# Performance work log

Hardware: AMD Instinct MI355X
Metric: run time of the kernel (lower is better)

## Reference

```python
import jax, jax.numpy as jnp
import numpy as np

B, T, P, D, H = 32, 64, 196, 768, 12
HD = D // H   # MHA head dim = 64
F = D // H    # GAT per-head out features = 64


def _grid_adj(num_patches):
    g = int(np.sqrt(num_patches))
    a = np.zeros((num_patches, num_patches), np.int32)
    for i in range(num_patches):
        a[i, i] = 1
        r, c = divmod(i, g)
        for dr in (-1, 0, 1):
            for dc in (-1, 0, 1):
                if dr == 0 and dc == 0:
                    continue
                nr, nc = r + dr, c + dc
                if 0 <= nr < g and 0 <= nc < g:
                    a[i, nr * g + nc] = 1
    return a


def setup_inputs():
    key = jax.random.key(0)
    ks = jax.random.split(key, 32)
    s = 0.02
    ta = jax.random.randint(ks[2], (B, T, T), 0, 2).astype(jnp.int32)
    ta = jnp.maximum(jnp.maximum(ta, ta.transpose(0, 2, 1)), jnp.eye(T, dtype=jnp.int32))
    return {
        'text_features': jax.random.normal(ks[0], (B, T, D), jnp.float32),
        'image_features': jax.random.normal(ks[1], (B, P, D), jnp.float32),
        'clip_text': jax.random.normal(ks[3], (B, 512), jnp.float32),
        'clip_image': jax.random.normal(ks[4], (B, 512), jnp.float32),
        'logit_scale': jnp.float32(4.6052),  # ln(100), CLIP default
        'wq': jax.random.normal(ks[5], (D, D), jnp.float32) * s,
        'bq': jnp.zeros((D,), jnp.float32),
        'wk': jax.random.normal(ks[6], (D, D), jnp.float32) * s,
        'bk': jnp.zeros((D,), jnp.float32),
        'wv': jax.random.normal(ks[7], (D, D), jnp.float32) * s,
        'bv': jnp.zeros((D,), jnp.float32),
        'wo': jax.random.normal(ks[8], (D, D), jnp.float32) * s,
        'bo': jnp.zeros((D,), jnp.float32),
        'Wt': jax.random.normal(ks[9], (D, H * F), jnp.float32) * s,
        'at': jax.random.normal(ks[10], (2 * F, 1), jnp.float32) * s,
        'Wi': jax.random.normal(ks[11], (D, H * F), jnp.float32) * s,
        'ai': jax.random.normal(ks[12], (2 * F, 1), jnp.float32) * s,
        'Wp': jax.random.normal(ks[13], (512, D), jnp.float32) * s,
        'bp': jnp.zeros((D,), jnp.float32),
        'f1w': jax.random.normal(ks[14], (3, 16), jnp.float32) * 0.3,
        'f1b': jnp.zeros((16,), jnp.float32),
        'f2w': jax.random.normal(ks[15], (16, 3), jnp.float32) * 0.3,
        'f2b': jnp.zeros((3,), jnp.float32),
        'c1w': jax.random.normal(ks[16], (D, D // 2), jnp.float32) * s,
        'c1b': jnp.zeros((D // 2,), jnp.float32),
        'c2w': jax.random.normal(ks[17], (D // 2, 2), jnp.float32) * s,
        'c2b': jnp.zeros((2,), jnp.float32),
        'text_adj': ta,
        'image_adj': jnp.asarray(_grid_adj(P)),
    }


def _gat(h, adj, W, a):
    # h: [N, D], adj: [N, N] (0/1), W: [D, H*F], a: [2F, 1]
    N = h.shape[0]
    Wh = (h @ W).reshape(N, H, F)
    # e_ij = leakyrelu(a^T [Wh_i ; Wh_j]) decomposed to avoid the N*N*2F concat tensor
    src = jnp.einsum('nhf,f->nh', Wh, a[:F, 0])   # [N, H]
    dst = jnp.einsum('nhf,f->nh', Wh, a[F:, 0])   # [N, H]
    e = jax.nn.leaky_relu(src[:, None, :] + dst[None, :, :], 0.2)  # [N, N, H]
    e = jnp.where(adj[:, :, None] > 0, e, jnp.float32(-9e15))
    att = jax.nn.softmax(e, axis=1)               # softmax over neighbors j
    hp = jnp.einsum('ijh,jhf->ihf', att, Wh)       # [N, H, F]
    return jax.nn.elu(hp.reshape(N, H * F))


def reference(text_features, image_features, clip_text, clip_image, logit_scale,
              wq, bq, wk, bk, wv, bv, wo, bo, Wt, at, Wi, ai, Wp, bp,
              f1w, f1b, f2w, f2b, c1w, c1b, c2w, c2b, text_adj, image_adj):
    # token-level cross attention (text queries, image keys/values)
    q = (text_features @ wq + bq).reshape(B, T, H, HD)
    k = (image_features @ wk + bk).reshape(B, P, H, HD)
    v = (image_features @ wv + bv).reshape(B, P, H, HD)
    scores = jnp.einsum('bthd,bphd->bhtp', q, k) / jnp.sqrt(jnp.float32(HD))
    upd = jnp.einsum('bhtp,bphd->bthd', jax.nn.softmax(scores, axis=-1), v)
    upd = upd.reshape(B, T, D) @ wo + bo           # [B, T, D]
    c = jnp.einsum('btd,bpd->btp', upd, image_features)
    s_token = jnp.mean(jnp.diagonal(c, axis1=-2, axis2=-1), axis=1)  # [B]
    f_token = upd.mean(axis=1)                     # [B, D]
    # per-sample GATs, batched via vmap
    tg = jax.vmap(lambda h, a_: _gat(h, a_, Wt, at))(text_features, text_adj)
    ig = jax.vmap(lambda h: _gat(h, image_adj, Wi, ai))(image_features)
    tgf = tg.mean(axis=1)
    igf = ig.mean(axis=1)

    def cos(x, y):
        nx = jnp.maximum(jnp.linalg.norm(x, axis=-1), 1e-8)
        ny = jnp.maximum(jnp.linalg.norm(y, axis=-1), 1e-8)
        return jnp.sum(x * y, axis=-1) / (nx * ny)

    s_phrase = cos(tgf, igf)
    s_global = jnp.exp(logit_scale) * cos(clip_text, clip_image)
    f_global = clip_text @ Wp + bp
    scores3 = jax.lax.stop_gradient(jnp.stack([s_token, s_phrase, s_global], axis=1))
    w = jax.nn.sigmoid(jax.nn.gelu(scores3 @ f1w + f1b, approximate=False) @ f2w + f2b)
    f_agg = w[:, 0:1] * f_token + w[:, 1:2] * tgf + w[:, 2:3] * f_global
    logits = jax.nn.relu(f_agg @ c1w + c1b) @ c2w + c2b  # dropout inactive (eval)
    return logits
```

## Files before the change

kernel.cpp:

```cpp
#include <hip/hip_runtime.h>
#include <hip/hip_bf16.h>
#include <math.h>

#define B 32
#define T 64
#define P 196
#define D 768
#define H 12

typedef __attribute__((ext_vector_type(8))) short short8;
typedef __attribute__((ext_vector_type(4))) float floatx4;

__device__ __forceinline__ float wave_sum(float v) {
#pragma unroll
  for (int o = 32; o > 0; o >>= 1) v += __shfl_xor(v, o);
  return v;
}
__device__ __forceinline__ unsigned short f2bf(float x) {
  unsigned u = __float_as_uint(x);
  u += 0x7FFFu + ((u >> 16) & 1u);
  return (unsigned short)(u >> 16);
}
__device__ __forceinline__ float bf2f(unsigned short x) {
  return __uint_as_float((unsigned)x << 16);
}
__device__ __forceinline__ float fexp(float x) { return __expf(x); }
__device__ __forceinline__ float frcp(float x) { return __builtin_amdgcn_rcpf(x); }
__device__ __forceinline__ void async_cp16(const unsigned short* g, unsigned short* l) {
  __builtin_amdgcn_global_load_lds(
      (const __attribute__((address_space(1))) unsigned int*)g,
      (__attribute__((address_space(3))) unsigned int*)l, 16, 0, 0);
}
__device__ __forceinline__ int xcd_remap(int orig, int nwg) {
  const int q = nwg >> 3, r = nwg & 7;
  const int x = orig & 7, o = orig >> 3;
  return (x < r ? x * (q + 1) : r * (q + 1) + (x - r) * q) + o;
}

struct WPack {
  const float* src[6];
  unsigned short* dst[6];
};
__global__ __launch_bounds__(256) void prep_kernel(
    WPack p,
    const float* __restrict__ text, unsigned short* __restrict__ text_bf, int n40,
    const float* __restrict__ img, unsigned short* __restrict__ img_bf, int n41,
    const float* __restrict__ bq, const float* __restrict__ bk,
    const float* __restrict__ bv,
    float* __restrict__ bt, float* __restrict__ bi, float* __restrict__ stok) {
  const int bid = blockIdx.x;
  if (bid < 3456) {
    __shared__ float tile[32][33];
    const int z = bid / 576, rem = bid % 576;
    const int bx = rem % 24, by = rem / 24;
    const float* W = p.src[z];
    unsigned short* Wt = p.dst[z];
    const int tx = threadIdx.x & 31, ty = threadIdx.x >> 5;
    const int n0 = bx * 32, k0 = by * 32;
#pragma unroll
    for (int r = 0; r < 4; ++r)
      tile[ty + 8 * r][tx] = W[(size_t)(k0 + ty + 8 * r) * D + n0 + tx];
    __syncthreads();
#pragma unroll
    for (int r = 0; r < 4; ++r)
      Wt[(size_t)(n0 + ty + 8 * r) * D + k0 + tx] = f2bf(tile[tx][ty + 8 * r]);
  } else if (bid < 9696) {
    int i = (bid - 3456) * 256 + threadIdx.x;
    const float* X;
    unsigned short* Y;
    int idx;
    if (i < n40) { X = text; Y = text_bf; idx = i; }
    else if (i < n40 + n41) { X = img; Y = img_bf; idx = i - n40; }
    else return;
    float4 vv = ((const float4*)X)[idx];
    ushort4 o;
    o.x = f2bf(vv.x); o.y = f2bf(vv.y); o.z = f2bf(vv.z); o.w = f2bf(vv.w);
    ((ushort4*)Y)[idx] = o;
  } else {
    int i = (bid - 9696) * 256 + threadIdx.x;
    if (i < 32) stok[i] = 0.f;
    if (i < 768) { bt[i] = bq[i]; bi[i] = bk[i]; }
    else if (i < 1536) { bt[i] = 0.f; bi[i] = bv[i - 768]; }
    else if (i < 2304) { bi[i] = 0.f; }
  }
}

struct GemmJob {
  const unsigned short* A;
  const unsigned short* Bt;
  const float* bias;
  void* C;
  int N, K, lda, ldb, colTiles;
};

template <bool BF16OUT>
__device__ __forceinline__ void gemm_body(const GemmJob& j, int bx, int by, int tid,
                                          char* smem) {
  unsigned short (*As)[128][32] = (unsigned short(*)[128][32])smem;
  unsigned short (*Bs)[128][32] = (unsigned short(*)[128][32])(smem + 24576);
  const int lane = tid & 63;
  const int w = tid >> 6;
  const int quad = lane >> 4;
  const int l15 = lane & 15;
  const int row0 = by * 128;
  const int col0 = bx * 128;
  const int m_off = (w & 1) * 64;
  const int n_off = (w >> 1) * 64;
  const int N = j.N, K = j.K;

  const int srow = 16 * w + (lane >> 2);
  const int scol = (((lane & 3) ^ ((lane >> 3) & 3))) * 8;
  const unsigned short* gA0 = j.A + (size_t)(row0 + srow) * j.lda + scol;
  const unsigned short* gA1 = j.A + (size_t)(row0 + srow + 64) * j.lda + scol;
  const unsigned short* gB0 = j.Bt + (size_t)(col0 + srow) * j.ldb + scol;
  const unsigned short* gB1 = j.Bt + (size_t)(col0 + srow + 64) * j.ldb + scol;

  const int rdc = (quad ^ ((l15 >> 1) & 3)) * 8;

  floatx4 acc[4][4] = {};
  short8 fA[4], fB_[4];
  short8 gA_[4], gB_[4];

#define STAGE(buf, kk)                                   \
  do {                                                   \
    async_cp16(gA0 + (kk), &As[buf][16 * w][0]);         \
    async_cp16(gA1 + (kk), &As[buf][64 + 16 * w][0]);    \
    async_cp16(gB0 + (kk), &Bs[buf][16 * w][0]);         \
    async_cp16(gB1 + (kk), &Bs[buf][64 + 16 * w][0]);    \
  } while (0)

  auto RD = [&](short8 (&AF)[4], short8 (&BF)[4], int buf) {
#pragma unroll
    for (int i = 0; i < 4; ++i)
      AF[i] = *(const short8*)&As[buf][m_off + 16 * i + l15][rdc];
#pragma unroll
    for (int j2 = 0; j2 < 4; ++j2)
      BF[j2] = *(const short8*)&Bs[buf][n_off + 16 * j2 + l15][rdc];
  };
  auto MM = [&](short8 (&AF)[4], short8 (&BF)[4]) {
#pragma unroll
    for (int i = 0; i < 4; ++i)
#pragma unroll
      for (int j2 = 0; j2 < 4; ++j2)
        acc[i][j2] = __builtin_amdgcn_mfma_f32_16x16x32_bf16(AF[i], BF[j2], acc[i][j2], 0, 0, 0);
  };
  auto PHASE = [&](short8 (&curA)[4], short8 (&curB)[4],
                   short8 (&nxtA)[4], short8 (&nxtB)[4],
                   int stageBuf, int readBuf, int kk) {
    if (kk + 64 < K) {
      STAGE(stageBuf, kk + 64);
      asm volatile("s_waitcnt vmcnt(4) lgkmcnt(0)" ::: "memory");
      __builtin_amdgcn_s_barrier();
      __builtin_amdgcn_sched_barrier(0);
      RD(nxtA, nxtB, readBuf);
    } else if (kk + 32 < K) {
      asm volatile("s_waitcnt vmcnt(0) lgkmcnt(0)" ::: "memory");
      __builtin_amdgcn_s_barrier();
      __builtin_amdgcn_sched_barrier(0);
      RD(nxtA, nxtB, readBuf);
    }
    MM(curA, curB);
  };

  STAGE(0, 0);
  STAGE(1, 32);
  asm volatile("s_waitcnt vmcnt(4)" ::: "memory");
  __builtin_amdgcn_s_barrier();
  __builtin_amdgcn_sched_barrier(0);
  RD(fA, fB_, 0);

  for (int k0 = 0; k0 < K; k0 += 192) {
    PHASE(fA, fB_, gA_, gB_, 2, 1, k0);
    PHASE(gA_, gB_, fA, fB_, 0, 2, k0 + 32);
    PHASE(fA, fB_, gA_, gB_, 1, 0, k0 + 64);
    PHASE(gA_, gB_, fA, fB_, 2, 1, k0 + 96);
    PHASE(fA, fB_, gA_, gB_, 0, 2, k0 + 128);
    PHASE(gA_, gB_, fA, fB_, 1, 0, k0 + 160);
  }
#undef STAGE

#pragma unroll
  for (int jj = 0; jj < 4; ++jj) {
    const int cg = col0 + n_off + 16 * jj + l15;
    const float bv = j.bias ? j.bias[cg] : 0.0f;
#pragma unroll
    for (int i = 0; i < 4; ++i) {
      const int rbase = row0 + m_off + 16 * i + quad * 4;
#pragma unroll
      for (int r = 0; r < 4; ++r) {
        const float val = acc[i][jj][r] + bv;
        const size_t idx = (size_t)(rbase + r) * N + cg;
        if (BF16OUT) ((unsigned short*)j.C)[idx] = f2bf(val);
        else ((float*)j.C)[idx] = val;
      }
    }
  }
}

__global__ __launch_bounds__(256) void gemm_mfma_dual_bf16(GemmJob j0, GemmJob j1,
                                                           int split, int total) {
  __shared__ __align__(16) char gsmem[49152];
  const bool first = ((int)blockIdx.x < split);
  const GemmJob& j = first ? j0 : j1;
  const int orig = first ? blockIdx.x : (blockIdx.x - split);
  const int bid = xcd_remap(orig, first ? split : total - split);
  const int bx = bid % j.colTiles;
  const int by = bid / j.colTiles;
  gemm_body<true>(j, bx, by, threadIdx.x, gsmem);
}


__device__ __forceinline__ void attn_body(
    char* smem, int h, int b,
    const unsigned short* __restrict__ qa, const unsigned short* __restrict__ kvw,
    unsigned short* __restrict__ attout) {
  const int tid = threadIdx.x, lane = tid & 63, w = tid >> 6;
  const int quad = lane >> 4, l15 = lane & 15;

  unsigned short (*Ks)[72] = (unsigned short(*)[72])smem;
  unsigned short (*Ps)[16][232] = (unsigned short(*)[16][232])smem;
  unsigned short (*VT)[232] = (unsigned short(*)[232])(smem + 29952);

  short8 aq[2];
#pragma unroll
  for (int ks = 0; ks < 2; ++ks)
    aq[ks] = *(const short8*)(qa + (size_t)(b * T + 16 * w + l15) * 1536 + h * 64 +
                              32 * ks + quad * 8);

  for (int i = tid; i < P * 8; i += 256) {
    const int p = i >> 3, dg = i & 7;
    const short8 k8 =
        *(const short8*)(kvw + (size_t)(b * P + p) * 2304 + h * 64 + dg * 8);
    *(short8*)&Ks[p][dg * 8] = k8;
  }
  {
    const int d = lane;
    const unsigned short* vbase = kvw + (size_t)b * P * 2304 + 768 + h * 64 + d;
    for (int pb = w; pb < 28; pb += 4) {
      short8 v;
#pragma unroll
      for (int z = 0; z < 8; ++z) {
        const int p = pb * 8 + z;
        v[z] = (p < P) ? (short)vbase[(size_t)p * 2304] : (short)0;
      }
      *(short8*)&VT[d][pb * 8] = v;
    }
  }
  __syncthreads();

  floatx4 sc[13];
#pragma unroll
  for (int tile = 0; tile < 13; ++tile) {
    int p = tile * 16 + l15;
    if (p > 195) p = 195;
    short8 bk0 = *(const short8*)&Ks[p][quad * 8];
    short8 bk1 = *(const short8*)&Ks[p][32 + quad * 8];
    floatx4 c = {};
    c = __builtin_amdgcn_mfma_f32_16x16x32_bf16(aq[0], bk0, c, 0, 0, 0);
    c = __builtin_amdgcn_mfma_f32_16x16x32_bf16(aq[1], bk1, c, 0, 0, 0);
    sc[tile] = c;
  }

  float mx[4] = {-3.4e38f, -3.4e38f, -3.4e38f, -3.4e38f};
#pragma unroll
  for (int tile = 0; tile < 13; ++tile)
#pragma unroll
    for (int r = 0; r < 4; ++r) {
      float s = sc[tile][r] * 0.125f;
      if (tile == 12 && l15 >= 4) s = -3.0e38f;
      sc[tile][r] = s;
      mx[r] = fmaxf(mx[r], s);
    }
#pragma unroll
  for (int off = 1; off < 16; off <<= 1)
#pragma unroll
    for (int r = 0; r < 4; ++r) mx[r] = fmaxf(mx[r], __shfl_xor(mx[r], off));

  float sm[4] = {};
#pragma unroll
  for (int tile = 0; tile < 13; ++tile)
#pragma unroll
    for (int r = 0; r < 4; ++r) {
      float e = fexp(sc[tile][r] - mx[r]);
      sc[tile][r] = e;
      sm[r] += e;
    }
#pragma unroll
  for (int off = 1; off < 16; off <<= 1)
#pragma unroll
    for (int r = 0; r < 4; ++r) sm[r] += __shfl_xor(sm[r], off);
  float inv[4];
#pragma unroll
  for (int r = 0; r < 4; ++r) inv[r] = frcp(sm[r]);

  __syncthreads();

#pragma unroll
  for (int tile = 0; tile < 13; ++tile)
#pragma unroll
    for (int r = 0; r < 4; ++r)
      Ps[w][quad * 4 + r][tile * 16 + l15] = f2bf(sc[tile][r]);
#pragma unroll
  for (int r = 0; r < 4; ++r)
    Ps[w][quad * 4 + r][208 + l15] = 0;

  floatx4 oc[4] = {};
#pragma unroll
  for (int ks = 0; ks < 7; ++ks) {
    short8 pa = *(const short8*)&Ps[w][l15][ks * 32 + quad * 8];
#pragma unroll
    for (int nt = 0; nt < 4; ++nt) {
      short8 bv = *(const short8*)&VT[nt * 16 + l15][ks * 32 + quad * 8];
      oc[nt] = __builtin_amdgcn_mfma_f32_16x16x32_bf16(pa, bv, oc[nt], 0, 0, 0);
    }
  }

#pragma unroll
  for (int nt = 0; nt < 4; ++nt)
#pragma unroll
    for (int r = 0; r < 4; ++r)
      attout[(size_t)(b * T + 16 * w + quad * 4 + r) * 768 + h * 64 + nt * 16 + l15] =
          f2bf(oc[nt][r] * inv[r]);
}

__global__ __launch_bounds__(256) void attn_kernel(
    const unsigned short* __restrict__ qa_bf, const unsigned short* __restrict__ kvw_bf,
    unsigned short* __restrict__ att_bf) {
  __shared__ __align__(16) char smem[59648];
  attn_body(smem, blockIdx.x, blockIdx.y, qa_bf, kvw_bf, att_bf);
}

__device__ __forceinline__ void text_gat_body(
    char* smem, int h, int b,
    const unsigned short* __restrict__ Wh, int ldw, const int* __restrict__ adj,
    const float* __restrict__ at, float* __restrict__ tgf) {
  const int tid = threadIdx.x, lane = tid & 63, w = tid >> 6;
  const int quad = lane >> 4, l15 = lane & 15;

  unsigned short (*VT)[72] = (unsigned short(*)[72])smem;
  unsigned short (*Ps)[16][72] = (unsigned short(*)[16][72])(smem + 9216);
  float* srcs = (float*)(smem + 18432);
  float* dsts = (float*)(smem + 18688);
  float (*redc)[64] = (float(*)[64])(smem + 18944);
  float* asv = (float*)(smem + 19968);
  float* adv = (float*)(smem + 20224);

  if (tid < 64) { asv[tid] = at[tid]; adv[tid] = at[64 + tid]; }
  {
    const int f = lane;
    const unsigned short* wbase = Wh + (size_t)(b * T) * ldw + h * 64 + f;
    for (int nb = w; nb < 8; nb += 4) {
      short8 v;
#pragma unroll
      for (int z = 0; z < 8; ++z)
        v[z] = (short)wbase[(size_t)(nb * 8 + z) * ldw];
      *(short8*)&VT[f][nb * 8] = v;
    }
  }
  __syncthreads();

  if (tid < 64) {
    float s = 0.f, dd = 0.f;
#pragma unroll 8
    for (int f = 0; f < 64; ++f) {
      const float wv = bf2f(VT[f][tid]);
      s += wv * asv[f];
      dd += wv * adv[f];
    }
    srcs[tid] = s;
    dsts[tid] = dd;
  }
  __syncthreads();

  const int i = 16 * w + l15;
  const float si = srcs[i];
  const int* ar = adj + (size_t)b * T * T + i * 64;
  float sm = 0.f;
#pragma unroll 8
  for (int jj = 0; jj < 16; ++jj) {
    const int j = 4 * jj + quad;
    float e = si + dsts[j];
    e = (e >= 0.f) ? e : 0.2f * e;
    const float p = (ar[j] != 0) ? fexp(e) : 0.f;
    sm += p;
    Ps[w][l15][j] = f2bf(p);
  }
  sm += __shfl_xor(sm, 16);
  sm += __shfl_xor(sm, 32);
  const float inv = frcp(sm);

  floatx4 oc[4] = {};
#pragma unroll
  for (int ks = 0; ks < 2; ++ks) {
    const short8 pa = *(const short8*)&Ps[w][l15][ks * 32 + quad * 8];
#pragma unroll
    for (int nt = 0; nt < 4; ++nt) {
      const short8 bv = *(const short8*)&VT[nt * 16 + l15][ks * 32 + quad * 8];
      oc[nt] = __builtin_amdgcn_mfma_f32_16x16x32_bf16(pa, bv, oc[nt], 0, 0, 0);
    }
  }

  float accd[4] = {};
#pragma unroll
  for (int r = 0; r < 4; ++r) {
    const float invr = __shfl(inv, quad * 4 + r);
#pragma unroll
    for (int nt = 0; nt < 4; ++nt) {
      const float hp = oc[nt][r] * invr;
      accd[nt] += (hp > 0.f) ? hp : (fexp(hp) - 1.0f);
    }
  }
#pragma unroll
  for (int nt = 0; nt < 4; ++nt) {
    accd[nt] += __shfl_xor(accd[nt], 16);
    accd[nt] += __shfl_xor(accd[nt], 32);
  }
  if (quad == 0) {
#pragma unroll
    for (int nt = 0; nt < 4; ++nt) redc[w][nt * 16 + l15] = accd[nt];
  }
  __syncthreads();
  if (w == 0) {
    const float tot = redc[0][lane] + redc[1][lane] + redc[2][lane] + redc[3][lane];
    tgf[b * D + h * 64 + lane] = tot * (1.0f / T);
  }
}

__device__ __forceinline__ void image_gat_body(
    char* smem, int h, int b,
    const unsigned short* __restrict__ Wh, int ldw, const float* __restrict__ ai,
    const int* __restrict__ adj, float* __restrict__ igf) {
  const int tid = threadIdx.x, lane = tid & 63, w = tid >> 6;
  const int quad = lane >> 4, l15 = lane & 15;

  unsigned short (*VT)[232] = (unsigned short(*)[232])smem;
  unsigned short (*Ps)[232] = (unsigned short(*)[232])(smem + 29696);
  float* srcs = (float*)(smem + 37120);
  float* dsts = (float*)(smem + 37904);
  float* asv = (float*)(smem + 38688);
  float* adv = (float*)(smem + 38944);

  if (tid < 64) { asv[tid] = ai[tid]; adv[tid] = ai[64 + tid]; }
  {
    const int f = lane;
    const unsigned short* wbase = Wh + (size_t)(b * P) * ldw + h * 64 + f;
    for (int nb = w; nb < 28; nb += 4) {
      short8 v;
#pragma unroll
      for (int z = 0; z < 8; ++z) {
        const int p = nb * 8 + z;
        v[z] = (p < P) ? (short)wbase[(size_t)p * ldw] : (short)0;
      }
      *(short8*)&VT[f][nb * 8] = v;
    }
  }
  __syncthreads();

  if (tid < P) {
    float s = 0.f, dd = 0.f;
#pragma unroll 8
    for (int f = 0; f < 64; ++f) {
      const float wv = bf2f(VT[f][tid]);
      s += wv * asv[f];
      dd += wv * adv[f];
    }
    srcs[tid] = s;
    dsts[tid] = dd;
  }
  __syncthreads();

  const int rloc = tid >> 4;
  const int cslot = tid & 15;
  float accw = 0.f;

  for (int tile = 0; tile < 13; ++tile) {
    const int i = tile * 16 + rloc;
    const int ii = (i < P) ? i : (P - 1);
    const float si = srcs[ii];
    const int* ar = adj + ii * P;
    int msk[13];
#pragma unroll
    for (int k = 0; k < 13; ++k) {
      const int jc = k * 16 + cslot;
      msk[k] = (jc < P) ? ar[jc] : 0;
    }
    float pvv[13];
    float sm = 0.f;
#pragma unroll
    for (int k = 0; k < 13; ++k) {
      const int jc = k * 16 + cslot;
      float p = 0.f;
      if (jc < P && msk[k] != 0) {
        float e = si + dsts[jc];
        e = (e >= 0.f) ? e : 0.2f * e;
        p = fexp(e);
      }
      pvv[k] = p;
      sm += p;
    }
    sm += __shfl_xor(sm, 1);
    sm += __shfl_xor(sm, 2);
    sm += __shfl_xor(sm, 4);
    sm += __shfl_xor(sm, 8);
    const float inv = frcp(sm);
#pragma unroll
    for (int k = 0; k < 13; ++k)
      Ps[rloc][k * 16 + cslot] = f2bf(pvv[k] * inv);
    Ps[rloc][208 + cslot] = 0;
    __syncthreads();

    floatx4 oc = {};
#pragma unroll
    for (int ks = 0; ks < 7; ++ks) {
      const short8 pa = *(const short8*)&Ps[l15][ks * 32 + quad * 8];
      const short8 bvv = *(const short8*)&VT[w * 16 + l15][ks * 32 + quad * 8];
      oc = __builtin_amdgcn_mfma_f32_16x16x32_bf16(pa, bvv, oc, 0, 0, 0);
    }
#pragma unroll
    for (int r = 0; r < 4; ++r) {
      const int io = tile * 16 + quad * 4 + r;
      if (io < P) {
        const float hp = oc[r];
        accw += (hp > 0.f) ? hp : (fexp(hp) - 1.0f);
      }
    }
    __syncthreads();
  }

  accw += __shfl_xor(accw, 16);
  accw += __shfl_xor(accw, 32);
  if (quad == 0)
    igf[b * D + h * 64 + w * 16 + l15] = accw * (1.0f / P);
}

__device__ __forceinline__ void fglob_body(
    char* smem, int jt, int b,
    const float* __restrict__ clip_t, const float* __restrict__ Wp,
    const float* __restrict__ bp, float* __restrict__ fglob) {
  const int j = threadIdx.x & 63, kc = threadIdx.x >> 6;
  float s = 0.f;
  const float* ct = clip_t + b * 512;
#pragma unroll 4
  for (int k = kc * 128; k < kc * 128 + 128; ++k)
    s += ct[k] * Wp[(size_t)k * D + jt * 64 + j];
  float (*red)[64] = (float(*)[64])smem;
  red[kc][j] = s;
  __syncthreads();
  if (kc == 0)
    fglob[b * D + jt * 64 + j] = red[0][j] + red[1][j] + red[2][j] + red[3][j] + bp[jt * 64 + j];
}

__global__ __launch_bounds__(256) void combo_kernel(
    GemmJob jwo0, GemmJob jwo1,
    const unsigned short* __restrict__ qa_bf,
    const int* __restrict__ text_adj, const float* __restrict__ at,
    float* __restrict__ tgf,
    const unsigned short* __restrict__ whi, int ldw_i,
    const float* __restrict__ ai, const int* __restrict__ image_adj,
    float* __restrict__ igf,
    const float* __restrict__ clip_t, const float* __restrict__ Wp,
    const float* __restrict__ bp, float* __restrict__ fglob) {
  __shared__ __align__(16) char smem[49152];
  const int bid = blockIdx.x;
  if (bid < 192) {
    const bool first = bid < 96;
    const GemmJob& j = first ? jwo0 : jwo1;
    const int orig = first ? bid : bid - 96;
    const int b2 = xcd_remap(orig, 96);
    gemm_body<false>(j, b2 % j.colTiles, b2 / j.colTiles, threadIdx.x, smem);
  } else if (bid < 576) {
    const int idx = bid - 192;
    text_gat_body(smem, idx % 12, idx / 12, qa_bf + 768, 1536, text_adj, at, tgf);
  } else if (bid < 960) {
    const int idx = bid - 576;
    image_gat_body(smem, idx % 12, idx / 12, whi, ldw_i, ai, image_adj, igf);
  } else {
    const int idx = bid - 960;
    fglob_body(smem, idx % 12, idx / 12, clip_t, Wp, bp, fglob);
  }
}

__global__ __launch_bounds__(256) void token_kernel(
    const float* __restrict__ upd0, const float* __restrict__ upd1,
    const float* __restrict__ img,
    float* __restrict__ f_token, float* __restrict__ s_token) {
  const int jt = blockIdx.x, b = blockIdx.y;
  const int l = threadIdx.x & 63, tg = threadIdx.x >> 6;
  const int d = jt * 64 + l;
  float fs = 0.f, ss = 0.f;
#pragma unroll 4
  for (int tt = 0; tt < 16; ++tt) {
    const int t = tg * 16 + tt;
    const size_t idx = (size_t)(b * T + t) * D + d;
    const float u = upd0[idx] + upd1[idx];
    fs += u;
    ss += u * img[(size_t)(b * P + t) * D + d];
  }
  __shared__ float red[4][64];
  __shared__ float sred[4];
  red[tg][l] = fs;
  const float sw = wave_sum(ss);
  if (l == 0) sred[tg] = sw;
  __syncthreads();
  if (tg == 0) {
    f_token[(size_t)b * D + d] =
        (red[0][l] + red[1][l] + red[2][l] + red[3][l]) * (1.0f / T);
    if (threadIdx.x == 0)
      atomicAdd(&s_token[b], (sred[0] + sred[1] + sred[2] + sred[3]) * (1.0f / T));
  }
}

__global__ __launch_bounds__(256) void xc1_kernel(
    const float* __restrict__ ftok, const float* __restrict__ tgf,
    const float* __restrict__ fglob, const float* __restrict__ c1w,
    float* __restrict__ Xc) {
  const int jt = blockIdx.x;
  const int r = blockIdx.y;
  const int b = r & 31, which = r >> 5;
  const float* src = (which == 0 ? ftok : which == 1 ? tgf : fglob) + (size_t)b * D;
  const int j = threadIdx.x & 63, kc = threadIdx.x >> 6;
  const int col = jt * 64 + j;
  float s = 0.f;
#pragma unroll 4
  for (int k = kc * 192; k < kc * 192 + 192; ++k)
    s += src[k] * c1w[(size_t)k * 384 + col];
  __shared__ float red[4][64];
  red[kc][j] = s;
  __syncthreads();
  if (kc == 0)
    Xc[(size_t)r * 384 + col] = red[0][j] + red[1][j] + red[2][j] + red[3][j];
}

__device__ __forceinline__ float block_sum(float v, float* red4) {
  v = wave_sum(v);
  __syncthreads();
  if ((threadIdx.x & 63) == 0) red4[threadIdx.x >> 6] = v;
  __syncthreads();
  return red4[0] + red4[1] + red4[2] + red4[3];
}

__global__ __launch_bounds__(256) void final_kernel(
    const float* __restrict__ tgf, const float* __restrict__ igf,
    const float* __restrict__ clip_t, const float* __restrict__ clip_i,
    const float* __restrict__ logit_scale, const float* __restrict__ s_token,
    const float* __restrict__ Xc,
    const float* __restrict__ f1w, const float* __restrict__ f1b,
    const float* __restrict__ f2w, const float* __restrict__ f2b,
    const float* __restrict__ c1b,
    const float* __restrict__ c2w, const float* __restrict__ c2b,
    float* __restrict__ out) {
  const int b = blockIdx.x, tid = threadIdx.x;
  __shared__ float red[4];
  __shared__ float sres[4];
  __shared__ float hid[384];

  float d0 = 0.f, d1 = 0.f, d2 = 0.f;
  for (int i = tid; i < D; i += 256) {
    float x = tgf[b * D + i], y = igf[b * D + i];
    d0 += x * y; d1 += x * x; d2 += y * y;
  }
  float dot_ti = block_sum(d0, red);
  float n_t = sqrtf(block_sum(d1, red));
  float n_i = sqrtf(block_sum(d2, red));
  float s_phrase = dot_ti / (fmaxf(n_t, 1e-8f) * fmaxf(n_i, 1e-8f));

  float c0 = 0.f, c1 = 0.f, c2 = 0.f;
  for (int i = tid; i < 512; i += 256) {
    float x = clip_t[b * 512 + i], y = clip_i[b * 512 + i];
    c0 += x * y; c1 += x * x; c2 += y * y;
  }
  float dc = block_sum(c0, red);
  float nt2 = sqrtf(block_sum(c1, red));
  float ni2 = sqrtf(block_sum(c2, red));
  float s_global = expf(logit_scale[0]) * dc / (fmaxf(nt2, 1e-8f) * fmaxf(ni2, 1e-8f));

  if (tid == 0) {
    float s3[3] = { s_token[b], s_phrase, s_global };
    float h1[16];
    for (int j = 0; j < 16; ++j) {
      float a = f1b[j];
      for (int i2 = 0; i2 < 3; ++i2) a += s3[i2] * f1w[i2 * 16 + j];
      h1[j] = 0.5f * a * (1.0f + erff(a * 0.70710678118654752f));
    }
    for (int j = 0; j < 3; ++j) {
      float a = f2b[j];
      for (int i2 = 0; i2 < 16; ++i2) a += h1[i2] * f2w[i2 * 3 + j];
      sres[j] = 1.0f / (1.0f + expf(-a));
    }
  }
  __syncthreads();
  const float w0 = sres[0], w1 = sres[1], w2 = sres[2];

  for (int j = tid; j < 384; j += 256) {
    const float a = w0 * Xc[(size_t)b * 384 + j] +
                    w1 * Xc[(size_t)(32 + b) * 384 + j] +
                    w2 * Xc[(size_t)(64 + b) * 384 + j] + c1b[j];
    hid[j] = fmaxf(a, 0.0f);
  }
  __syncthreads();

  float p0 = 0.f, p1 = 0.f;
  for (int k2 = tid; k2 < 384; k2 += 256) {
    p0 += hid[k2] * c2w[k2 * 2 + 0];
    p1 += hid[k2] * c2w[k2 * 2 + 1];
  }
  p0 = block_sum(p0, red);
  p1 = block_sum(p1, red);
  if (tid == 0) {
    out[b * 2 + 0] = p0 + c2b[0];
    out[b * 2 + 1] = p1 + c2b[1];
  }
}

extern "C" void kernel_launch(void* const* d_in, const int* in_sizes, int n_in,
                              void* d_out, int out_size, void* d_ws, size_t ws_size,
                              hipStream_t stream) {
  const float* text   = (const float*)d_in[0];
  const float* img    = (const float*)d_in[1];
  const float* clip_t = (const float*)d_in[2];
  const float* clip_i = (const float*)d_in[3];
  const float* lscale = (const float*)d_in[4];
  const float* wq = (const float*)d_in[5];
  const float* bq = (const float*)d_in[6];
  const float* wk = (const float*)d_in[7];
  const float* bk = (const float*)d_in[8];
  const float* wv = (const float*)d_in[9];
  const float* bv = (const float*)d_in[10];
  const float* wo = (const float*)d_in[11];
  const float* bo = (const float*)d_in[12];
  const float* Wt = (const float*)d_in[13];
  const float* at = (const float*)d_in[14];
  const float* Wi = (const float*)d_in[15];
  const float* ai = (const float*)d_in[16];
  const float* Wp = (const float*)d_in[17];
  const float* bp = (const float*)d_in[18];
  const float* f1w = (const float*)d_in[19];
  const float* f1b = (const float*)d_in[20];
  const float* f2w = (const float*)d_in[21];
  const float* f2b = (const float*)d_in[22];
  const float* c1w = (const float*)d_in[23];
  const float* c1b = (const float*)d_in[24];
  const float* c2w = (const float*)d_in[25];
  const float* c2b = (const float*)d_in[26];
  const int* text_adj  = (const int*)d_in[27];
  const int* image_adj = (const int*)d_in[28];
  float* out = (float*)d_out;

  const size_t nTD = (size_t)B * T * D;
  const size_t nPD = (size_t)B * P * D;
  const size_t nWW = (size_t)D * D;

  float* fbuf = (float*)d_ws;
  size_t o = 0;
  float* upd0    = fbuf + o; o += nTD;
  float* upd1    = fbuf + o; o += nTD;
  float* ftok    = fbuf + o; o += (size_t)B * D;
  float* stok    = fbuf + o; o += 32;
  float* tgf     = fbuf + o; o += (size_t)B * D;
  float* igf     = fbuf + o; o += (size_t)B * D;
  float* fglob   = fbuf + o; o += (size_t)B * D;
  float* bcat_t  = fbuf + o; o += 1536;
  float* bcat_i3 = fbuf + o; o += 2304;
  float* Xc      = fbuf + o; o += (size_t)96 * 384;
  unsigned short* sbuf = (unsigned short*)(fbuf + o);
  size_t so = 0;
  unsigned short* kvw_bf    = sbuf + so; so += 3 * nPD;
  unsigned short* qa_bf     = sbuf + so; so += 2 * nTD;
  unsigned short* text_bf   = sbuf + so; so += nTD;
  unsigned short* img_bf    = sbuf + so; so += nPD;
  unsigned short* att_bf    = sbuf + so; so += nTD;
  unsigned short* wcat_txt  = sbuf + so; so += 2 * nWW;
  unsigned short* wcat_img3 = sbuf + so; so += 3 * nWW;
  unsigned short* wo_t      = sbuf + so; so += nWW;

  WPack wp;
  wp.src[0] = wq; wp.dst[0] = wcat_txt;
  wp.src[1] = Wt; wp.dst[1] = wcat_txt + nWW;
  wp.src[2] = wk; wp.dst[2] = wcat_img3;
  wp.src[3] = wv; wp.dst[3] = wcat_img3 + nWW;
  wp.src[4] = Wi; wp.dst[4] = wcat_img3 + 2 * nWW;
  wp.src[5] = wo; wp.dst[5] = wo_t;
  {
    const int n40 = (int)(nTD / 4), n41 = (int)(nPD / 4);
    prep_kernel<<<9708, 256, 0, stream>>>(wp, text, text_bf, n40, img, img_bf, n41,
                                          bq, bk, bv, bcat_t, bcat_i3, stok);
  }

  const int MT = B * T;
  const int MP = B * P;

  GemmJob jimg;
  jimg.A = img_bf; jimg.Bt = wcat_img3; jimg.bias = bcat_i3; jimg.C = kvw_bf;
  jimg.N = 2304; jimg.K = D; jimg.lda = D; jimg.ldb = D; jimg.colTiles = 2304 / 128;
  GemmJob jtxt;
  jtxt.A = text_bf; jtxt.Bt = wcat_txt; jtxt.bias = bcat_t; jtxt.C = qa_bf;
  jtxt.N = 1536; jtxt.K = D; jtxt.lda = D; jtxt.ldb = D; jtxt.colTiles = 1536 / 128;
  const int splitBlocks = (2304 / 128) * (MP / 128);
  const int totalBlocks = splitBlocks + (1536 / 128) * (MT / 128);
  gemm_mfma_dual_bf16<<<totalBlocks, 256, 0, stream>>>(jimg, jtxt, splitBlocks, totalBlocks);

  attn_kernel<<<dim3(H, B), 256, 0, stream>>>(qa_bf, kvw_bf, att_bf);

  GemmJob jwo0;
  jwo0.A = att_bf; jwo0.Bt = wo_t; jwo0.bias = bo; jwo0.C = upd0;
  jwo0.N = D; jwo0.K = 384; jwo0.lda = D; jwo0.ldb = D; jwo0.colTiles = D / 128;
  GemmJob jwo1;
  jwo1.A = att_bf + 384; jwo1.Bt = wo_t + 384; jwo1.bias = nullptr; jwo1.C = upd1;
  jwo1.N = D; jwo1.K = 384; jwo1.lda = D; jwo1.ldb = D; jwo1.colTiles = D / 128;
  const unsigned short* whi_bf = kvw_bf + 1536;
  combo_kernel<<<1344, 256, 0, stream>>>(
      jwo0, jwo1,
      qa_bf, text_adj, at, tgf,
      whi_bf, 2304, ai, image_adj, igf,
      clip_t, Wp, bp, fglob);

  token_kernel<<<dim3(12, B), 256, 0, stream>>>(upd0, upd1, img, ftok, stok);
  xc1_kernel<<<dim3(6, 96), 256, 0, stream>>>(ftok, tgf, fglob, c1w, Xc);
  final_kernel<<<B, 256, 0, stream>>>(tgf, igf, clip_t, clip_i, lscale, stok, Xc,
                                      f1w, f1b, f2w, f2b, c1b, c2w, c2b, out);
}
```

Measured before the change: 263.0 us.

## Fuse token mean and diagonal score into output-projection GEMM epilogue

The output projection GEMM epilogue no longer writes the two partial fp32 result buffers. It reduces the mean over tokens and the diagonal dot product with image features directly, and accumulates both into f_token and s_token with atomics. This removes the separate token kernel launch and the global round trip of two [B,T,D] fp32 buffers, and ftok is now zeroed in the prep kernel. The fglob and xc1 dot-product loops are also split into four independent accumulators to expose ILP. The trade-off is atomic contention on ftok/stok and float summation order that is no longer deterministic.

```diff
diff --git a/kernel.cpp b/kernel.cpp
--- a/kernel.cpp
+++ b/kernel.cpp
@@ -47,7 +47,8 @@
     const float* __restrict__ img, unsigned short* __restrict__ img_bf, int n41,
     const float* __restrict__ bq, const float* __restrict__ bk,
     const float* __restrict__ bv,
-    float* __restrict__ bt, float* __restrict__ bi, float* __restrict__ stok) {
+    float* __restrict__ bt, float* __restrict__ bi, float* __restrict__ stok,
+    float* __restrict__ ftok) {
   const int bid = blockIdx.x;
   if (bid < 3456) {
     __shared__ float tile[32][33];
@@ -78,6 +79,7 @@
     ((ushort4*)Y)[idx] = o;
   } else {
     int i = (bid - 9696) * 256 + threadIdx.x;
+    ftok[i] = 0.f;
     if (i < 32) stok[i] = 0.f;
     if (i < 768) { bt[i] = bq[i]; bi[i] = bk[i]; }
     else if (i < 1536) { bt[i] = 0.f; bi[i] = bv[i - 768]; }
@@ -93,9 +95,11 @@
   int N, K, lda, ldb, colTiles;
 };
 
-template <bool BF16OUT>
+template <bool BF16OUT, bool TOKEN>
 __device__ __forceinline__ void gemm_body(const GemmJob& j, int bx, int by, int tid,
-                                          char* smem) {
+                                          char* smem,
+                                          const float* timg, float* ftok,
+                                          float* stok) {
   unsigned short (*As)[128][32] = (unsigned short(*)[128][32])smem;
   unsigned short (*Bs)[128][32] = (unsigned short(*)[128][32])(smem + 24576);
   const int lane = tid & 63;
@@ -179,19 +183,43 @@
   }
 #undef STAGE
 
-#pragma unroll
-  for (int jj = 0; jj < 4; ++jj) {
-    const int cg = col0 + n_off + 16 * jj + l15;
-    const float bv = j.bias ? j.bias[cg] : 0.0f;
-#pragma unroll
-    for (int i = 0; i < 4; ++i) {
-      const int rbase = row0 + m_off + 16 * i + quad * 4;
-#pragma unroll
-      for (int r = 0; r < 4; ++r) {
-        const float val = acc[i][jj][r] + bv;
-        const size_t idx = (size_t)(rbase + r) * N + cg;
-        if (BF16OUT) ((unsigned short*)j.C)[idx] = f2bf(val);
-        else ((float*)j.C)[idx] = val;
+  if constexpr (TOKEN) {
+    const int bb = (row0 + m_off) >> 6;
+    float sval = 0.f;
+#pragma unroll
+    for (int jj = 0; jj < 4; ++jj) {
+      const int cg = col0 + n_off + 16 * jj + l15;
+      const float bv = j.bias ? j.bias[cg] : 0.0f;
+      float fsum = 0.f;
+#pragma unroll
+      for (int i = 0; i < 4; ++i) {
+#pragma unroll
+        for (int r = 0; r < 4; ++r) {
+          const float val = acc[i][jj][r] + bv;
+          const int t = 16 * i + quad * 4 + r;
+          fsum += val;
+          sval += val * timg[(size_t)(bb * P + t) * D + cg];
+        }
+      }
+      atomicAdd(&ftok[(size_t)bb * D + cg], fsum * (1.0f / T));
+    }
+    const float sv = wave_sum(sval);
+    if (lane == 0) atomicAdd(&stok[bb], sv * (1.0f / T));
+  } else {
+#pragma unroll
+    for (int jj = 0; jj < 4; ++jj) {
+      const int cg = col0 + n_off + 16 * jj + l15;
+      const float bv = j.bias ? j.bias[cg] : 0.0f;
+#pragma unroll
+      for (int i = 0; i < 4; ++i) {
+        const int rbase = row0 + m_off + 16 * i + quad * 4;
+#pragma unroll
+        for (int r = 0; r < 4; ++r) {
+          const float val = acc[i][jj][r] + bv;
+          const size_t idx = (size_t)(rbase + r) * N + cg;
+          if (BF16OUT) ((unsigned short*)j.C)[idx] = f2bf(val);
+          else ((float*)j.C)[idx] = val;
+        }
       }
     }
   }
@@ -206,7 +234,7 @@
   const int bid = xcd_remap(orig, first ? split : total - split);
   const int bx = bid % j.colTiles;
   const int by = bid / j.colTiles;
-  gemm_body<true>(j, bx, by, threadIdx.x, gsmem);
+  gemm_body<true, false>(j, bx, by, threadIdx.x, gsmem, nullptr, nullptr, nullptr);
 }
 
 
@@ -538,13 +566,18 @@
     const float* __restrict__ clip_t, const float* __restrict__ Wp,
     const float* __restrict__ bp, float* __restrict__ fglob) {
   const int j = threadIdx.x & 63, kc = threadIdx.x >> 6;
-  float s = 0.f;
-  const float* ct = clip_t + b * 512;
-#pragma unroll 4
-  for (int k = kc * 128; k < kc * 128 + 128; ++k)
-    s += ct[k] * Wp[(size_t)k * D + jt * 64 + j];
+  const float* ct = clip_t + b * 512 + kc * 128;
+  const float* wp = Wp + (size_t)(kc * 128) * D + jt * 64 + j;
+  float s0 = 0.f, s1 = 0.f, s2 = 0.f, s3 = 0.f;
+#pragma unroll
+  for (int k = 0; k < 128; k += 4) {
+    s0 += ct[k]     * wp[(size_t)k * D];
+    s1 += ct[k + 1] * wp[(size_t)(k + 1) * D];
+    s2 += ct[k + 2] * wp[(size_t)(k + 2) * D];
+    s3 += ct[k + 3] * wp[(size_t)(k + 3) * D];
+  }
   float (*red)[64] = (float(*)[64])smem;
-  red[kc][j] = s;
+  red[kc][j] = (s0 + s1) + (s2 + s3);
   __syncthreads();
   if (kc == 0)
     fglob[b * D + jt * 64 + j] = red[0][j] + red[1][j] + red[2][j] + red[3][j] + bp[jt * 64 + j];
@@ -552,6 +585,7 @@
 
 __global__ __launch_bounds__(256) void combo_kernel(
     GemmJob jwo0, GemmJob jwo1,
+    const float* __restrict__ timg, float* __restrict__ ftok, float* __restrict__ stok,
     const unsigned short* __restrict__ qa_bf,
     const int* __restrict__ text_adj, const float* __restrict__ at,
     float* __restrict__ tgf,
@@ -567,7 +601,8 @@
     const GemmJob& j = first ? jwo0 : jwo1;
     const int orig = first ? bid : bid - 96;
     const int b2 = xcd_remap(orig, 96);
-    gemm_body<false>(j, b2 % j.colTiles, b2 / j.colTiles, threadIdx.x, smem);
+    gemm_body<false, true>(j, b2 % j.colTiles, b2 / j.colTiles, threadIdx.x, smem,
+                           timg, ftok, stok);
   } else if (bid < 576) {
     const int idx = bid - 192;
     text_gat_body(smem, idx % 12, idx / 12, qa_bf + 768, 1536, text_adj, at, tgf);
@@ -577,36 +612,6 @@
   } else {
     const int idx = bid - 960;
     fglob_body(smem, idx % 12, idx / 12, clip_t, Wp, bp, fglob);
-  }
-}
-
-__global__ __launch_bounds__(256) void token_kernel(
-    const float* __restrict__ upd0, const float* __restrict__ upd1,
-    const float* __restrict__ img,
-    float* __restrict__ f_token, float* __restrict__ s_token) {
-  const int jt = blockIdx.x, b = blockIdx.y;
-  const int l = threadIdx.x & 63, tg = threadIdx.x >> 6;
-  const int d = jt * 64 + l;
-  float fs = 0.f, ss = 0.f;
-#pragma unroll 4
-  for (int tt = 0; tt < 16; ++tt) {
-    const int t = tg * 16 + tt;
-    const size_t idx = (size_t)(b * T + t) * D + d;
-    const float u = upd0[idx] + upd1[idx];
-    fs += u;
-    ss += u * img[(size_t)(b * P + t) * D + d];
-  }
-  __shared__ float red[4][64];
-  __shared__ float sred[4];
-  red[tg][l] = fs;
-  const float sw = wave_sum(ss);
-  if (l == 0) sred[tg] = sw;
-  __syncthreads();
-  if (tg == 0) {
-    f_token[(size_t)b * D + d] =
-        (red[0][l] + red[1][l] + red[2][l] + red[3][l]) * (1.0f / T);
-    if (threadIdx.x == 0)
-      atomicAdd(&s_token[b], (sred[0] + sred[1] + sred[2] + sred[3]) * (1.0f / T));
   }
 }
 
@@ -620,12 +625,18 @@
   const float* src = (which == 0 ? ftok : which == 1 ? tgf : fglob) + (size_t)b * D;
   const int j = threadIdx.x & 63, kc = threadIdx.x >> 6;
   const int col = jt * 64 + j;
-  float s = 0.f;
-#pragma unroll 4
-  for (int k = kc * 192; k < kc * 192 + 192; ++k)
-    s += src[k] * c1w[(size_t)k * 384 + col];
+  const float* cw = c1w + (size_t)(kc * 192) * 384 + col;
+  const float* sk = src + kc * 192;
+  float s0 = 0.f, s1 = 0.f, s2 = 0.f, s3 = 0.f;
+#pragma unroll 12
+  for (int k = 0; k < 192; k += 4) {
+    s0 += sk[k]     * cw[(size_t)k * 384];
+    s1 += sk[k + 1] * cw[(size_t)(k + 1) * 384];
+    s2 += sk[k + 2] * cw[(size_t)(k + 2) * 384];
+    s3 += sk[k + 3] * cw[(size_t)(k + 3) * 384];
+  }
   __shared__ float red[4][64];
-  red[kc][j] = s;
+  red[kc][j] = (s0 + s1) + (s2 + s3);
   __syncthreads();
   if (kc == 0)
     Xc[(size_t)r * 384 + col] = red[0][j] + red[1][j] + red[2][j] + red[3][j];
@@ -752,8 +763,6 @@
 
   float* fbuf = (float*)d_ws;
   size_t o = 0;
-  float* upd0    = fbuf + o; o += nTD;
-  float* upd1    = fbuf + o; o += nTD;
   float* ftok    = fbuf + o; o += (size_t)B * D;
   float* stok    = fbuf + o; o += 32;
   float* tgf     = fbuf + o; o += (size_t)B * D;
@@ -782,8 +791,8 @@
   wp.src[5] = wo; wp.dst[5] = wo_t;
   {
     const int n40 = (int)(nTD / 4), n41 = (int)(nPD / 4);
-    prep_kernel<<<9708, 256, 0, stream>>>(wp, text, text_bf, n40, img, img_bf, n41,
-                                          bq, bk, bv, bcat_t, bcat_i3, stok);
+    prep_kernel<<<9792, 256, 0, stream>>>(wp, text, text_bf, n40, img, img_bf, n41,
+                                          bq, bk, bv, bcat_t, bcat_i3, stok, ftok);
   }
 
   const int MT = B * T;
@@ -802,19 +811,18 @@
   attn_kernel<<<dim3(H, B), 256, 0, stream>>>(qa_bf, kvw_bf, att_bf);
 
   GemmJob jwo0;
-  jwo0.A = att_bf; jwo0.Bt = wo_t; jwo0.bias = bo; jwo0.C = upd0;
+  jwo0.A = att_bf; jwo0.Bt = wo_t; jwo0.bias = bo; jwo0.C = nullptr;
   jwo0.N = D; jwo0.K = 384; jwo0.lda = D; jwo0.ldb = D; jwo0.colTiles = D / 128;
   GemmJob jwo1;
-  jwo1.A = att_bf + 384; jwo1.Bt = wo_t + 384; jwo1.bias = nullptr; jwo1.C = upd1;
+  jwo1.A = att_bf + 384; jwo1.Bt = wo_t + 384; jwo1.bias = nullptr; jwo1.C = nullptr;
   jwo1.N = D; jwo1.K = 384; jwo1.lda = D; jwo1.ldb = D; jwo1.colTiles = D / 128;
   const unsigned short* whi_bf = kvw_bf + 1536;
   combo_kernel<<<1344, 256, 0, stream>>>(
-      jwo0, jwo1,
+      jwo0, jwo1, img, ftok, stok,
       qa_bf, text_adj, at, tgf,
       whi_bf, 2304, ai, image_adj, igf,
       clip_t, Wp, bp, fglob);
 
-  token_kernel<<<dim3(12, B), 256, 0, stream>>>(upd0, upd1, img, ftok, stok);
   xc1_kernel<<<dim3(6, 96), 256, 0, stream>>>(ftok, tgf, fglob, c1w, Xc);
   final_kernel<<<B, 256, 0, stream>>>(tgf, igf, clip_t, clip_i, lscale, stok, Xc,
                                       f1w, f1b, f2w, f2b, c1b, c2w, c2b, out);
```

After: 251.4 us (median of 2 runs). 4.4% less time.
